# Optimization experiments

Hardware: AMD Instinct MI355X
Metric: run time of the kernel (lower is better)

The kernel has to match this reference:

```python
import jax, jax.numpy as jnp
import numpy as np

E = 100000          # number of edges
IN_FEATS = 256      # in_edge_feats
HIDDEN = 128        # hidden_size
K = 16              # neighbors per edge (uniform-degree rendering of ragged lists)


def setup_inputs() -> dict:
    key = jax.random.key(0)
    k1, k2, k3, k4 = jax.random.split(key, 4)
    edge_feats = jax.random.normal(k1, (E, IN_FEATS), dtype=jnp.float32)
    neighbors = jax.random.randint(k2, (E, K), 0, E, dtype=jnp.int32)
    # Linear params (torch Linear: y = x @ W^T + b; here W stored as [in, out])
    W = jax.random.normal(k3, (IN_FEATS, HIDDEN), dtype=jnp.float32) / np.sqrt(IN_FEATS)
    b = jax.random.normal(k4, (HIDDEN,), dtype=jnp.float32) * 0.01
    return {"edge_feats": edge_feats, "neighbors": neighbors, "W": W, "b": b}


def reference(edge_feats, neighbors, W, b):
    # Dense linear transform of all edge features: [E, H]
    t = edge_feats @ W + b
    # Gather each edge's K neighbor transformed features and sum: [E, K, H] -> [E, H]
    nbr_sum = jnp.take(t, neighbors, axis=0).sum(axis=1)
    # agg[i] = t[i] + sum_{n in neighbors[i]} t[n]
    return t + nbr_sum
```

## Files before the change

kernel.cpp:

```cpp
#include <hip/hip_runtime.h>
#include <hip/hip_bf16.h>
#include <stdint.h>

#define E_EDGES 100000
#define IN_F    256
#define HID     128
#define KNB     16
#define NCHUNK  ((E_EDGES + 63) / 64)
#define GEMM_GRID 512

typedef short bf16x8 __attribute__((ext_vector_type(8)));
typedef float f32x4  __attribute__((ext_vector_type(4)));

__device__ __forceinline__ unsigned short f2bf(float f) {
    union { float f; unsigned u; } v; v.f = f;
    unsigned u = v.u;
    u += 0x7fffu + ((u >> 16) & 1u);
    return (unsigned short)(u >> 16);
}

__global__ void conv_w_kernel(const float* __restrict__ W, unsigned short* __restrict__ Wtf) {
    int d = blockIdx.x * 256 + threadIdx.x;
    int f = d >> 6, L = d & 63;
    int k0 = f >> 3, ct = f & 7, quad = L >> 4, l15 = L & 15;
    int n  = ct * 16 + l15;
    int kb = (k0 * 4 + quad) * 8;
    const float* wp = W + (size_t)kb * HID + n;
    unsigned short h[8];
    #pragma unroll
    for (int j = 0; j < 8; ++j) h[j] = f2bf(wp[(size_t)j * HID]);
    uint4 o;
    o.x = (unsigned)h[0] | ((unsigned)h[1] << 16);
    o.y = (unsigned)h[2] | ((unsigned)h[3] << 16);
    o.z = (unsigned)h[4] | ((unsigned)h[5] << 16);
    o.w = (unsigned)h[6] | ((unsigned)h[7] << 16);
    *(uint4*)(Wtf + (size_t)d * 8) = o;
}

__launch_bounds__(256, 2)
__global__ void gemm_t_kernel(const float* __restrict__ A,
                              const unsigned short* __restrict__ Wtf,
                              const float* __restrict__ bias,
                              unsigned short* __restrict__ T) {
    __shared__ unsigned short Bs[32768];
    const int tid  = threadIdx.x;
    const int wave = tid >> 6;
    const int lane = tid & 63;
    const int l15  = lane & 15;
    const int quad = lane >> 4;

    int c = blockIdx.x;
    int arow = c * 64 + wave * 16 + l15;
    if (arow >= E_EDGES) arow = E_EDGES - 1;
    const float* ap = A + (size_t)arow * IN_F + quad * 8;
    float4 af32[16];
    #pragma unroll
    for (int k0 = 0; k0 < 8; ++k0) {
        af32[2 * k0]     = *(const float4*)(ap + k0 * 32);
        af32[2 * k0 + 1] = *(const float4*)(ap + k0 * 32 + 4);
    }

    #pragma unroll
    for (int it = 0; it < 16; ++it) {
        int d = it * 256 + tid;
        *(uint4*)(Bs + (size_t)d * 8) = *(const uint4*)(Wtf + (size_t)d * 8);
    }

    float4 bv4[8];
    #pragma unroll
    for (int ct = 0; ct < 8; ++ct)
        bv4[ct] = *(const float4*)(bias + ct * 16 + quad * 4);

    __syncthreads();

    for (; c < NCHUNK; c += GEMM_GRID) {
        bf16x8 apre[8];
        #pragma unroll
        for (int k0 = 0; k0 < 8; ++k0) {
            float4 lo = af32[2 * k0], hi = af32[2 * k0 + 1];
            bf16x8 f;
            f[0] = (short)f2bf(lo.x); f[1] = (short)f2bf(lo.y);
            f[2] = (short)f2bf(lo.z); f[3] = (short)f2bf(lo.w);
            f[4] = (short)f2bf(hi.x); f[5] = (short)f2bf(hi.y);
            f[6] = (short)f2bf(hi.z); f[7] = (short)f2bf(hi.w);
            apre[k0] = f;
        }

        {
            int cn = c + GEMM_GRID;
            int arow2 = cn * 64 + wave * 16 + l15;
            if (arow2 >= E_EDGES) arow2 = E_EDGES - 1;
            const float* ap2 = A + (size_t)arow2 * IN_F + quad * 8;
            #pragma unroll
            for (int k0 = 0; k0 < 8; ++k0) {
                af32[2 * k0]     = *(const float4*)(ap2 + k0 * 32);
                af32[2 * k0 + 1] = *(const float4*)(ap2 + k0 * 32 + 4);
            }
        }
        __builtin_amdgcn_sched_barrier(0);

        f32x4 acc[8] = {};
        #pragma unroll
        for (int k0 = 0; k0 < 8; ++k0) {
            #pragma unroll
            for (int ct = 0; ct < 8; ++ct) {
                bf16x8 bf = *(const bf16x8*)(Bs + ((size_t)((k0 * 8 + ct) * 64 + lane)) * 8);
                acc[ct] = __builtin_amdgcn_mfma_f32_16x16x32_bf16(bf, apre[k0], acc[ct], 0, 0, 0);
            }
        }

        const int row = c * 64 + wave * 16 + l15;
        if (row < E_EDGES) {
            unsigned short* tp = T + (size_t)row * HID + quad * 4;
            #pragma unroll
            for (int ct = 0; ct < 8; ++ct) {
                unsigned short h0 = f2bf(acc[ct][0] + bv4[ct].x);
                unsigned short h1 = f2bf(acc[ct][1] + bv4[ct].y);
                unsigned short h2 = f2bf(acc[ct][2] + bv4[ct].z);
                unsigned short h3 = f2bf(acc[ct][3] + bv4[ct].w);
                uint2 o;
                o.x = (unsigned)h0 | ((unsigned)h1 << 16);
                o.y = (unsigned)h2 | ((unsigned)h3 << 16);
                *(uint2*)(tp + ct * 16) = o;
            }
        }
    }
}

__launch_bounds__(256)
__global__ void gather_sum_kernel(const unsigned short* __restrict__ T,
                                  const int* __restrict__ nbr,
                                  float* __restrict__ out) {
    __shared__ int sidx[256];
    const int tid   = threadIdx.x;
    const int edge0 = blockIdx.x * 16;
    sidx[tid] = nbr[(size_t)edge0 * KNB + tid];
    __syncthreads();

    const int el   = tid >> 4;
    const int lane = tid & 15;
    const int edge = edge0 + el;

    const unsigned short* tb = T + (size_t)lane * 8;
    uint4 v[17];
    v[0] = *(const uint4*)(tb + (size_t)edge * HID);
    #pragma unroll
    for (int k = 0; k < KNB; ++k)
        v[k + 1] = *(const uint4*)(tb + (size_t)sidx[el * KNB + k] * HID);
    __builtin_amdgcn_sched_barrier(0);

    float acc[8] = {};
    #pragma unroll
    for (int k = 0; k < 17; ++k) {
        unsigned w[4] = { v[k].x, v[k].y, v[k].z, v[k].w };
        union { unsigned u; float f; } c;
        #pragma unroll
        for (int j = 0; j < 4; ++j) {
            c.u = w[j] << 16;          acc[2 * j]     += c.f;
            c.u = w[j] & 0xffff0000u;  acc[2 * j + 1] += c.f;
        }
    }

    float* op = out + (size_t)edge * HID + lane * 8;
    float4 o0 = { acc[0], acc[1], acc[2], acc[3] };
    float4 o1 = { acc[4], acc[5], acc[6], acc[7] };
    *(float4*)op       = o0;
    *(float4*)(op + 4) = o1;
}

extern "C" void kernel_launch(void* const* d_in, const int* in_sizes, int n_in,
                              void* d_out, int out_size, void* d_ws, size_t ws_size,
                              hipStream_t stream) {
    const float* edge_feats = (const float*)d_in[0];
    const int*   neighbors  = (const int*)d_in[1];
    const float* W          = (const float*)d_in[2];
    const float* b          = (const float*)d_in[3];
    float*       out        = (float*)d_out;

    unsigned short* Wtf = (unsigned short*)d_ws;
    unsigned short* T   = (unsigned short*)d_ws + (size_t)IN_F * HID;

    conv_w_kernel<<<16, 256, 0, stream>>>(W, Wtf);
    gemm_t_kernel<<<GEMM_GRID, 256, 0, stream>>>(edge_feats, Wtf, b, T);
    gather_sum_kernel<<<E_EDGES / 16, 256, 0, stream>>>(T, neighbors, out);
}
```

Before: 230.2 us.

## Slice-sort neighbor indices and gather in row-slice order for cache locality

Each gather block now handles 128 edges. It bucket-sorts every edge's neighbor indices (plus the edge itself) into 16 row slices in shared memory, then all edges walk the slices together. The aim is to concentrate concurrent gathers in one region of T so they hit in cache. The cost is serial dependent loads within each slice, fewer loads in flight, and extra shared-memory sorting work per block.

```diff
diff --git a/kernel.cpp b/kernel.cpp
--- a/kernel.cpp
+++ b/kernel.cpp
@@ -8,6 +8,12 @@
 #define KNB     16
 #define NCHUNK  ((E_EDGES + 63) / 64)
 #define GEMM_GRID 512
+
+#define NS          16
+#define SLICE_ROWS  6250
+#define GCHUNKS     8
+#define EDGES_PER_BLK (GCHUNKS * 16)
+#define GATHER_GRID ((E_EDGES + EDGES_PER_BLK - 1) / EDGES_PER_BLK)
 
 typedef short bf16x8 __attribute__((ext_vector_type(8)));
 typedef float f32x4  __attribute__((ext_vector_type(4)));
@@ -127,45 +133,115 @@
     }
 }
 
-__launch_bounds__(256)
+__device__ __forceinline__ void acc_bf16x8(float a[8], uint4 v) {
+    unsigned w[4] = { v.x, v.y, v.z, v.w };
+    union { unsigned u; float f; } c;
+    #pragma unroll
+    for (int j = 0; j < 4; ++j) {
+        c.u = w[j] << 16;          a[2 * j]     += c.f;
+        c.u = w[j] & 0xffff0000u;  a[2 * j + 1] += c.f;
+    }
+}
+
+__launch_bounds__(256, 4)
 __global__ void gather_sum_kernel(const unsigned short* __restrict__ T,
                                   const int* __restrict__ nbr,
                                   float* __restrict__ out) {
-    __shared__ int sidx[256];
+    __shared__ int sidx[EDGES_PER_BLK * 16];
+    __shared__ int ssort[EDGES_PER_BLK * 17];
+    __shared__ int soff[EDGES_PER_BLK * 17];
+    __shared__ int scur[EDGES_PER_BLK * 17];
+
     const int tid   = threadIdx.x;
-    const int edge0 = blockIdx.x * 16;
-    sidx[tid] = nbr[(size_t)edge0 * KNB + tid];
+    const int edge0 = blockIdx.x * EDGES_PER_BLK;
+    const int el    = tid >> 4;
+    const int lane  = tid & 15;
+
+    {
+        int g = edge0 * KNB + tid * 8;
+        if (g > E_EDGES * KNB - 8) g = E_EDGES * KNB - 8;
+        const uint4* np = (const uint4*)(nbr + g);
+        *(uint4*)(sidx + tid * 8)     = np[0];
+        *(uint4*)(sidx + tid * 8 + 4) = np[1];
+    }
     __syncthreads();
 
-    const int el   = tid >> 4;
-    const int lane = tid & 15;
-    const int edge = edge0 + el;
-
-    const unsigned short* tb = T + (size_t)lane * 8;
-    uint4 v[17];
-    v[0] = *(const uint4*)(tb + (size_t)edge * HID);
-    #pragma unroll
-    for (int k = 0; k < KNB; ++k)
-        v[k + 1] = *(const uint4*)(tb + (size_t)sidx[el * KNB + k] * HID);
-    __builtin_amdgcn_sched_barrier(0);
-
-    float acc[8] = {};
-    #pragma unroll
-    for (int k = 0; k < 17; ++k) {
-        unsigned w[4] = { v[k].x, v[k].y, v[k].z, v[k].w };
-        union { unsigned u; float f; } c;
-        #pragma unroll
-        for (int j = 0; j < 4; ++j) {
-            c.u = w[j] << 16;          acc[2 * j]     += c.f;
-            c.u = w[j] & 0xffff0000u;  acc[2 * j + 1] += c.f;
-        }
-    }
-
-    float* op = out + (size_t)edge * HID + lane * 8;
-    float4 o0 = { acc[0], acc[1], acc[2], acc[3] };
-    float4 o1 = { acc[4], acc[5], acc[6], acc[7] };
-    *(float4*)op       = o0;
-    *(float4*)(op + 4) = o1;
+    if (tid < EDGES_PER_BLK) {
+        const int t = tid;
+        unsigned self = (unsigned)(edge0 + t);
+        if (self > E_EDGES - 1) self = E_EDGES - 1;
+
+        #pragma unroll
+        for (int s = 0; s < NS; ++s) scur[t * 17 + s] = 0;
+        #pragma unroll
+        for (int k = 0; k < KNB; ++k) {
+            unsigned idx = (unsigned)sidx[t * 16 + k];
+            scur[t * 17 + idx / SLICE_ROWS] += 1;
+        }
+        scur[t * 17 + self / SLICE_ROWS] += 1;
+
+        int run = 0;
+        soff[t * 17 + 0] = 0;
+        #pragma unroll
+        for (int s = 0; s < NS; ++s) {
+            run += scur[t * 17 + s];
+            soff[t * 17 + s + 1] = run;
+        }
+        #pragma unroll
+        for (int s = 0; s < NS; ++s) scur[t * 17 + s] = soff[t * 17 + s];
+
+        #pragma unroll
+        for (int k = 0; k < KNB; ++k) {
+            unsigned idx = (unsigned)sidx[t * 16 + k];
+            int s = idx / SLICE_ROWS;
+            ssort[t * 17 + scur[t * 17 + s]++] = (int)idx;
+        }
+        {
+            int s = self / SLICE_ROWS;
+            ssort[t * 17 + scur[t * 17 + s]++] = (int)self;
+        }
+    }
+    __syncthreads();
+
+    const unsigned short* Tb = T + (size_t)lane * 8;
+
+    float acc[GCHUNKS][8] = {};
+    int   cur[GCHUNKS];
+    #pragma unroll
+    for (int c = 0; c < GCHUNKS; ++c) cur[c] = 0;
+
+    for (int s = 0; s < NS; ++s) {
+        #pragma unroll
+        for (int c = 0; c < GCHUNKS; ++c) {
+            const int e   = c * 16 + el;
+            int j         = cur[c];
+            const int end = soff[e * 17 + s + 1];
+            cur[c] = end;
+            if (j < end) {
+                int idx = ssort[e * 17 + j];
+                uint4 v = *(const uint4*)(Tb + (size_t)idx * HID);
+                for (++j; j < end; ++j) {
+                    int idx2 = ssort[e * 17 + j];
+                    uint4 v2 = *(const uint4*)(Tb + (size_t)idx2 * HID);
+                    acc_bf16x8(acc[c], v);
+                    v = v2;
+                }
+                acc_bf16x8(acc[c], v);
+            }
+        }
+    }
+
+    #pragma unroll
+    for (int c = 0; c < GCHUNKS; ++c) {
+        const int edge = edge0 + c * 16 + el;
+        if (edge < E_EDGES) {
+            float* op = out + (size_t)edge * HID + lane * 8;
+            float4 o0 = { acc[c][0], acc[c][1], acc[c][2], acc[c][3] };
+            float4 o1 = { acc[c][4], acc[c][5], acc[c][6], acc[c][7] };
+            *(float4*)op       = o0;
+            *(float4*)(op + 4) = o1;
+        }
+    }
 }
 
 extern "C" void kernel_launch(void* const* d_in, const int* in_sizes, int n_in,
@@ -182,5 +258,5 @@
 
     conv_w_kernel<<<16, 256, 0, stream>>>(W, Wtf);
     gemm_t_kernel<<<GEMM_GRID, 256, 0, stream>>>(edge_feats, Wtf, b, T);
-    gather_sum_kernel<<<E_EDGES / 16, 256, 0, stream>>>(T, neighbors, out);
-}
+    gather_sum_kernel<<<GATHER_GRID, 256, 0, stream>>>(T, neighbors, out);
+}
```

Result: slower. 279.6 us (+21.5%).

## Sort gather indices by row slice to localize neighbor reads in cache

Applied to the files above, without the earlier changes.

Each gather block now handles 80 edges. Per edge, a counting sort in shared memory buckets the 17 row indices (16 neighbors plus self) into 16 slices of T. All edges in the block then walk the slices in the same order, so concurrent gathers hit a narrower address range and should reuse L2/MALL better. Outputs are written with nontemporal stores. In exchange the loads become serial data-dependent loops with shared-memory indirection and branch divergence, which reduces memory-level parallelism compared with the previous 17 independent loads in flight.

```diff
diff --git a/kernel.cpp b/kernel.cpp
--- a/kernel.cpp
+++ b/kernel.cpp
@@ -8,6 +8,12 @@
 #define KNB     16
 #define NCHUNK  ((E_EDGES + 63) / 64)
 #define GEMM_GRID 512
+
+#define NS          16
+#define SLICE_ROWS  6250
+#define GCHUNKS     5
+#define EDGES_PER_BLK (GCHUNKS * 16)
+#define GATHER_GRID (E_EDGES / EDGES_PER_BLK)
 
 typedef short bf16x8 __attribute__((ext_vector_type(8)));
 typedef float f32x4  __attribute__((ext_vector_type(4)));
@@ -127,45 +133,121 @@
     }
 }
 
-__launch_bounds__(256)
+__device__ __forceinline__ float u2f(unsigned u) {
+    union { unsigned u; float f; } c; c.u = u; return c.f;
+}
+__device__ __forceinline__ f32x4 declo(uint4 v) {
+    f32x4 r = { u2f(v.x << 16), u2f(v.x & 0xffff0000u),
+                u2f(v.y << 16), u2f(v.y & 0xffff0000u) };
+    return r;
+}
+__device__ __forceinline__ f32x4 dechi(uint4 v) {
+    f32x4 r = { u2f(v.z << 16), u2f(v.z & 0xffff0000u),
+                u2f(v.w << 16), u2f(v.w & 0xffff0000u) };
+    return r;
+}
+
+__launch_bounds__(256, 5)
 __global__ void gather_sum_kernel(const unsigned short* __restrict__ T,
                                   const int* __restrict__ nbr,
                                   float* __restrict__ out) {
-    __shared__ int sidx[256];
+    __shared__ int ssort[EDGES_PER_BLK * 17];
+    __shared__ int soff[EDGES_PER_BLK * 17];
+    __shared__ int scur[EDGES_PER_BLK * 17];
+
     const int tid   = threadIdx.x;
-    const int edge0 = blockIdx.x * 16;
-    sidx[tid] = nbr[(size_t)edge0 * KNB + tid];
+    const int edge0 = blockIdx.x * EDGES_PER_BLK;
+    const int el    = tid >> 4;
+    const int lane  = tid & 15;
+
+    if (tid < EDGES_PER_BLK) {
+        const int t = tid;
+        const unsigned self = (unsigned)(edge0 + t);
+        const int* np = nbr + (size_t)(edge0 + t) * KNB;
+
+        unsigned idxs[KNB];
+        #pragma unroll
+        for (int k = 0; k < KNB; k += 4) {
+            uint4 q = *(const uint4*)(np + k);
+            idxs[k] = q.x; idxs[k + 1] = q.y; idxs[k + 2] = q.z; idxs[k + 3] = q.w;
+        }
+
+        #pragma unroll
+        for (int s = 0; s < NS; ++s) scur[t * 17 + s] = 0;
+        #pragma unroll
+        for (int k = 0; k < KNB; ++k)
+            scur[t * 17 + idxs[k] / SLICE_ROWS] += 1;
+        scur[t * 17 + self / SLICE_ROWS] += 1;
+
+        int run = 0;
+        #pragma unroll
+        for (int s = 0; s < NS; ++s) {
+            int c0 = scur[t * 17 + s];
+            soff[t * 17 + s] = run;
+            scur[t * 17 + s] = run;
+            run += c0;
+        }
+        soff[t * 17 + NS] = run;
+
+        #pragma unroll
+        for (int k = 0; k < KNB; ++k) {
+            int s = (int)(idxs[k] / SLICE_ROWS);
+            ssort[t * 17 + scur[t * 17 + s]++] = (int)idxs[k];
+        }
+        {
+            int s = (int)(self / SLICE_ROWS);
+            ssort[t * 17 + scur[t * 17 + s]++] = (int)self;
+        }
+    }
     __syncthreads();
 
-    const int el   = tid >> 4;
-    const int lane = tid & 15;
-    const int edge = edge0 + el;
-
-    const unsigned short* tb = T + (size_t)lane * 8;
-    uint4 v[17];
-    v[0] = *(const uint4*)(tb + (size_t)edge * HID);
-    #pragma unroll
-    for (int k = 0; k < KNB; ++k)
-        v[k + 1] = *(const uint4*)(tb + (size_t)sidx[el * KNB + k] * HID);
-    __builtin_amdgcn_sched_barrier(0);
-
-    float acc[8] = {};
-    #pragma unroll
-    for (int k = 0; k < 17; ++k) {
-        unsigned w[4] = { v[k].x, v[k].y, v[k].z, v[k].w };
-        union { unsigned u; float f; } c;
-        #pragma unroll
-        for (int j = 0; j < 4; ++j) {
-            c.u = w[j] << 16;          acc[2 * j]     += c.f;
-            c.u = w[j] & 0xffff0000u;  acc[2 * j + 1] += c.f;
-        }
-    }
-
-    float* op = out + (size_t)edge * HID + lane * 8;
-    float4 o0 = { acc[0], acc[1], acc[2], acc[3] };
-    float4 o1 = { acc[4], acc[5], acc[6], acc[7] };
-    *(float4*)op       = o0;
-    *(float4*)(op + 4) = o1;
+    const unsigned short* Tb = T + (size_t)lane * 8;
+
+#define DECL_CHUNK(c) \
+    f32x4 accL##c = {0.f, 0.f, 0.f, 0.f}; \
+    f32x4 accH##c = {0.f, 0.f, 0.f, 0.f}; \
+    int   cur##c  = 0; \
+    const int base##c = (c * 16 + el) * 17;
+
+    DECL_CHUNK(0) DECL_CHUNK(1) DECL_CHUNK(2) DECL_CHUNK(3) DECL_CHUNK(4)
+#undef DECL_CHUNK
+
+#define RUN_CHUNK(c) { \
+    const int e_ = soff[base##c + s + 1]; \
+    int j_ = cur##c; \
+    cur##c = e_; \
+    if (j_ < e_) { \
+        int idx_ = ssort[base##c + j_]; \
+        uint4 v_ = *(const uint4*)(Tb + (size_t)idx_ * HID); \
+        for (++j_; j_ < e_; ++j_) { \
+            int idx2_ = ssort[base##c + j_]; \
+            uint4 v2_ = *(const uint4*)(Tb + (size_t)idx2_ * HID); \
+            accL##c += declo(v_); \
+            accH##c += dechi(v_); \
+            v_ = v2_; \
+        } \
+        accL##c += declo(v_); \
+        accH##c += dechi(v_); \
+    } }
+
+    for (int s = 0; s < NS; ++s) {
+        RUN_CHUNK(0)
+        RUN_CHUNK(1)
+        RUN_CHUNK(2)
+        RUN_CHUNK(3)
+        RUN_CHUNK(4)
+    }
+#undef RUN_CHUNK
+
+#define STORE_CHUNK(c) { \
+    const int edge_ = edge0 + c * 16 + el; \
+    float* op_ = out + (size_t)edge_ * HID + lane * 8; \
+    __builtin_nontemporal_store(accL##c, (f32x4*)op_); \
+    __builtin_nontemporal_store(accH##c, (f32x4*)(op_ + 4)); \
+    }
+
+    STORE_CHUNK(0) STORE_CHUNK(1) STORE_CHUNK(2) STORE_CHUNK(3) STORE_CHUNK(4)
+#undef STORE_CHUNK
 }
 
 extern "C" void kernel_launch(void* const* d_in, const int* in_sizes, int n_in,
@@ -182,5 +264,5 @@
 
     conv_w_kernel<<<16, 256, 0, stream>>>(W, Wtf);
     gemm_t_kernel<<<GEMM_GRID, 256, 0, stream>>>(edge_feats, Wtf, b, T);
-    gather_sum_kernel<<<E_EDGES / 16, 256, 0, stream>>>(T, neighbors, out);
-}
+    gather_sum_kernel<<<GATHER_GRID, 256, 0, stream>>>(T, neighbors, out);
+}
```

New measurement: 248.0 us. 7.7% more time.
